# Kernel tuning notes

Measured on AMD Instinct MI355X. Metric: run time of the kernel, lower is better.

## Reference

```python
import jax, jax.numpy as jnp
import numpy as np

B = 50000      # batch of graphs
NOBJ = 7       # tangram pieces per graph
HID = 64
EMB = 32
SIGMA = 25.0   # VE-SDE sigma for marginal_prob_std


def _lin_init(k, fin, fout):
    kw, kb = jax.random.split(k)
    s = 1.0 / np.sqrt(fin)
    w = jax.random.uniform(kw, (fin, fout), minval=-s, maxval=s, dtype=jnp.float32)
    b = jax.random.uniform(kb, (fout,), minval=-s, maxval=s, dtype=jnp.float32)
    return w, b


def setup_inputs() -> dict:
    key = jax.random.key(0)
    ks = jax.random.split(key, 16)
    N = B * NOBJ
    omega = jax.random.normal(ks[0], (N, 3), dtype=jnp.float32)
    t = jax.random.uniform(ks[1], (B, 1), minval=1e-3, maxval=1.0, dtype=jnp.float32)
    # fully-connected edges (no self loops) per graph, offset by graph index
    a, b = np.meshgrid(np.arange(NOBJ), np.arange(NOBJ), indexing='ij')
    m = a != b
    src0, dst0 = a[m], b[m]                       # (42,)
    offs = (np.arange(B) * NOBJ)[:, None]         # (B,1)
    src = (src0[None, :] + offs).reshape(-1)
    dst = (dst0[None, :] + offs).reshape(-1)
    edge_index = jnp.asarray(np.stack([src, dst]), dtype=jnp.int32)  # (2, B*42)
    W_fourier = jax.random.normal(ks[2], (EMB // 2,), dtype=jnp.float32) * 30.0
    wi1, bi1 = _lin_init(ks[3], 3, HID)
    wi2, bi2 = _lin_init(ks[4], HID, HID)
    wt, bt = _lin_init(ks[5], EMB, EMB)
    w1a, b1a = _lin_init(ks[6], HID * 2, HID)
    w1b, b1b = _lin_init(ks[7], HID, HID)
    w2a, b2a = _lin_init(ks[8], (HID + EMB) * 2, HID)
    w2b, b2b = _lin_init(ks[9], HID, HID)
    w3a, b3a = _lin_init(ks[10], (HID + EMB) * 2, HID)
    w3b, b3b = _lin_init(ks[11], HID, 3)
    return dict(omega=omega, edge_index=edge_index, t=t, num_objs=NOBJ,
                W_fourier=W_fourier,
                wi1=wi1, bi1=bi1, wi2=wi2, bi2=bi2, wt=wt, bt=bt,
                w1a=w1a, b1a=b1a, w1b=w1b, b1b=b1b,
                w2a=w2a, b2a=b2a, w2b=w2b, b2b=b2b,
                w3a=w3a, b3a=b3a, w3b=w3b, b3b=b3b)


def _mlp(x, wa, ba, wb, bb):
    return jax.nn.relu(x @ wa + ba) @ wb + bb


def reference(omega, edge_index, t, num_objs, W_fourier,
              wi1, bi1, wi2, bi2, wt, bt,
              w1a, b1a, w1b, b1b, w2a, b2a, w2b, b2b, w3a, b3a, w3b, b3b):
    N = omega.shape[0]
    src, dst = edge_index[0], edge_index[1]

    def edge_conv(x, wa, ba, wb, bb):
        # EdgeConv: msg = mlp([x_i, x_j - x_i]); max-aggregate at target i
        xi = x[dst]
        msg = _mlp(jnp.concatenate([xi, x[src] - xi], axis=-1), wa, ba, wb, bb)
        return jax.ops.segment_max(msg, dst, num_segments=N)

    init_feature = _mlp(omega, wi1, bi1, wi2, bi2)          # (N, HID)
    # Gaussian Fourier time embedding -> ReLU -> Linear -> ReLU
    proj = t[:, 0][:, None] * W_fourier[None, :] * (2.0 * jnp.pi)   # (B, EMB/2)
    emb = jnp.concatenate([jnp.sin(proj), jnp.cos(proj)], axis=-1)  # (B, EMB)
    xs = jax.nn.relu(jax.nn.relu(emb) @ wt + bt)                    # (B, EMB)
    # torch: xs.repeat(1, num_objs, 1).view(B*num_objs, -1) == tile whole block
    x_sigma = jnp.tile(xs, (num_objs, 1))                           # (N, EMB)

    x = jax.nn.relu(edge_conv(init_feature, w1a, b1a, w1b, b1b))
    x = jnp.concatenate([x, x_sigma], axis=-1)
    x = jax.nn.relu(edge_conv(x, w2a, b2a, w2b, b2b))
    x = jnp.concatenate([x, x_sigma], axis=-1)
    x = edge_conv(x, w3a, b3a, w3b, b3b)                            # (N, 3)

    # torch: t.repeat(1, num_objs).view(B*num_objs, -1) == repeat_interleave
    t_r = jnp.repeat(t, num_objs, axis=0)                           # (N, 1)
    std = jnp.sqrt((SIGMA ** (2.0 * t_r) - 1.0) / (2.0 * jnp.log(SIGMA)))
    return x / (std + 1e-7)
```

## Files before the change

### kernel.cpp

```cpp
#include <hip/hip_runtime.h>


#define NB 50000

typedef unsigned short u16;
typedef unsigned int u32;
typedef short short8 __attribute__((ext_vector_type(8)));
typedef float f32x4 __attribute__((ext_vector_type(4)));
typedef unsigned int u32x4 __attribute__((ext_vector_type(4)));

#define OFF_I  0
#define OFF_1A 8192
#define OFF_2A 24576
#define OFF_3A 49152
#define OFF_1B 73728
#define OFF_2B 81920
#define OFF_WT 90112
#define OFF_3B 92160

#define HSTR 144
#define HLO  2304
#define PQS  304
#define SOFF 8512
#define SSTR 264
#define WREG 12736

__device__ __forceinline__ float b2f(u16 u) {
    return __uint_as_float(((u32)u) << 16);
}
__device__ __forceinline__ u16 f2b(float f) {
    u32 u = __float_as_uint(f);
    u += 0x7FFFu + ((u >> 16) & 1u);
    return (u16)(u >> 16);
}
__device__ __forceinline__ void split2(float v, u16& h, u16& l) {
    u32 u = __float_as_uint(v);
    h = (u16)(u >> 16);
    float d = v - __uint_as_float(u & 0xffff0000u);
    l = f2b(d);
}
__device__ __forceinline__ float bcast(float v, int l) {
    return __uint_as_float(__builtin_amdgcn_readlane(__float_as_uint(v), l));
}

__global__ __launch_bounds__(128) void pack_kernel(
    const float* __restrict__ wi2, const float* __restrict__ w1a,
    const float* __restrict__ w2a, const float* __restrict__ w3a,
    const float* __restrict__ w1b, const float* __restrict__ w2b,
    const float* __restrict__ wt,  const float* __restrict__ w3b,
    u16* __restrict__ ws)
{
    int blk = blockIdx.x;
    int j    = blockIdx.y;
    int half = threadIdx.x >> 6;
    int lane = threadIdx.x & 63;
    float v;
    u16* dst;
    if (blk < 88) {
        const float* src; int NT, qoff, obase, frag;
        if (blk < 8)       { src = wi2; NT = 4; qoff = 0;  obase = OFF_I;  frag = blk;      }
        else if (blk < 24) { src = w1a; NT = 8; qoff = 64; obase = OFF_1A; frag = blk - 8;  }
        else if (blk < 48) { src = w2a; NT = 8; qoff = 96; obase = OFF_2A; frag = blk - 24; }
        else if (blk < 72) { src = w3a; NT = 8; qoff = 96; obase = OFF_3A; frag = blk - 48; }
        else if (blk < 80) { src = w1b; NT = 4; qoff = 0;  obase = OFF_1B; frag = blk - 72; }
        else               { src = w2b; NT = 4; qoff = 0;  obase = OFF_2B; frag = blk - 80; }
        int kt = frag / NT, nt = frag % NT;
        int k = kt * 32 + (lane >> 4) * 8 + j;
        int n = nt * 16 + (lane & 15);
        int idx = (n < 64) ? (k * 64 + n) : ((qoff + k) * 64 + (n - 64));
        v = src[idx];
        dst = ws + obase + frag * 1024 + half * 512 + lane * 8 + j;
    } else if (blk < 90) {
        int frag = blk - 88;
        int k = (lane >> 4) * 8 + j;
        int n = frag * 16 + (lane & 15);
        v = wt[k * 32 + n];
        dst = ws + OFF_WT + frag * 1024 + half * 512 + lane * 8 + j;
    } else {
        int frag = blk - 90;
        int k = frag * 32 + (lane >> 4) * 8 + j;
        int n = lane & 15;
        v = (n < 3) ? w3b[k * 3 + n] : 0.f;
        dst = ws + OFF_3B + frag * 1024 + half * 512 + lane * 8 + j;
    }
    u16 hi = f2b(v);
    *dst = (half == 0) ? hi : f2b(v - b2f(hi));
}

__device__ __forceinline__ f32x4 mfma1(short8 a, short8 b, f32x4 acc) {
    return __builtin_amdgcn_mfma_f32_16x16x32_bf16(a, b, acc, 0, 0, 0);
}
__device__ __forceinline__ f32x4 mfma3(short8 ah, short8 al, short8 bh, short8 bl, f32x4 acc) {
    acc = mfma1(ah, bh, acc);
    acc = mfma1(ah, bl, acc);
    acc = mfma1(al, bh, acc);
    return acc;
}

#define ROW(k) ((k) < 7 ? (k) : (k) + 1)

__device__ __forceinline__ void putX(char* G, int k, int L, float v) {
    int r = ROW(k);
    u16 h, l;
    split2(v, h, l);
    *(u16*)(G + r * HSTR + L * 2) = h;
    *(u16*)(G + HLO + r * HSTR + L * 2) = l;
}
__device__ __forceinline__ void loadA2(const char* G, int L, short8* Ah, short8* Al) {
#pragma unroll
    for (int kt = 0; kt < 2; ++kt) {
        Ah[kt] = *(const short8*)(G + (L & 15) * HSTR + kt * 64 + (L >> 4) * 16);
        Al[kt] = *(const short8*)(G + HLO + (L & 15) * HSTR + kt * 64 + (L >> 4) * 16);
    }
}
template<int KT, int NT>
__device__ __forceinline__ void lin_pass(const u16* __restrict__ ws, int off, int nt0,
                                         const short8* Ah, const short8* Al,
                                         char* Sg, int L) {
#pragma unroll
    for (int ntc = 0; ntc < 4; ++ntc) {
        f32x4 a1 = {0.f, 0.f, 0.f, 0.f}, a2 = {0.f, 0.f, 0.f, 0.f};
#pragma unroll
        for (int kt = 0; kt < KT; ++kt) {
            int f = kt * NT + nt0 + ntc;
            short8 bh = *(const short8*)(ws + off + f * 1024 + L * 8);
            short8 bl = *(const short8*)(ws + off + f * 1024 + 512 + L * 8);
            a1 = mfma1(Ah[kt], bh, a1);
            a2 = mfma1(Ah[kt], bl, a2);
            a2 = mfma1(Al[kt], bh, a2);
        }
#pragma unroll
        for (int rr = 0; rr < 4; ++rr)
            *(float*)(Sg + ((L >> 4) * 4 + rr) * SSTR + ntc * 64 + (L & 15) * 4) = a1[rr] + a2[rr];
    }
}
__device__ __forceinline__ void copyQ(char* PQ, const char* Sb, int L) {
#pragma unroll
    for (int k = 0; k < 14; ++k)
        *(float*)(PQ + (14 + k) * PQS + L * 4) =
            *(const float*)(Sb + ROW(k) * SSTR + L * 4);
}
__device__ __forceinline__ void fixP(char* PQ, const char* Sb, float vb, int L) {
#pragma unroll
    for (int k = 0; k < 14; ++k) {
        float p = *(const float*)(Sb + ROW(k) * SSTR + L * 4);
        float q = *(const float*)(PQ + (14 + k) * PQS + L * 4);
        *(float*)(PQ + k * PQS + L * 4) = p + vb - q;
    }
}
__device__ __forceinline__ void pack2(float a, float b, u32& H, u32& Lo) {
    u32 ua = __float_as_uint(a), ub = __float_as_uint(b);
    H = __builtin_amdgcn_perm(ub, ua, 0x07060302);
    float da = a - __uint_as_float(ua & 0xffff0000u);
    float db = b - __uint_as_float(ub & 0xffff0000u);
    u32 r;
    asm("v_cvt_pk_bf16_f32 %0, %1, %2" : "=v"(r) : "v"(da), "v"(db));
    Lo = r;
}
__device__ __forceinline__ void buildA1(const char* bp, const char* bq,
                                        short8& Ah, short8& Al) {
    f32x4 p0 = *(const f32x4*)bp,  p1 = *(const f32x4*)(bp + 16);
    f32x4 q0 = *(const f32x4*)bq,  q1 = *(const f32x4*)(bq + 16);
    float h0 = fmaxf(p0[0] + q0[0], 0.f), h1 = fmaxf(p0[1] + q0[1], 0.f);
    float h2 = fmaxf(p0[2] + q0[2], 0.f), h3 = fmaxf(p0[3] + q0[3], 0.f);
    float h4 = fmaxf(p1[0] + q1[0], 0.f), h5 = fmaxf(p1[1] + q1[1], 0.f);
    float h6 = fmaxf(p1[2] + q1[2], 0.f), h7 = fmaxf(p1[3] + q1[3], 0.f);
    u32 H0, H1, H2, H3, L0, L1, L2, L3;
    pack2(h0, h1, H0, L0);
    pack2(h2, h3, H1, L1);
    pack2(h4, h5, H2, L2);
    pack2(h6, h7, H3, L3);
    u32x4 Hv = {H0, H1, H2, H3};
    u32x4 Lv = {L0, L1, L2, L3};
    Ah = __builtin_bit_cast(short8, Hv);
    Al = __builtin_bit_cast(short8, Lv);
}
__device__ __forceinline__ void buildA(const char* PQ, int c, int L,
                                       short8& Ah0, short8& Al0,
                                       short8& Ah1, short8& Al1) {
    int e  = c * 16 + (L & 15);
    int gb = (e >= 42) ? 1 : 0;
    int el = e - gb * 42;
    int i  = el / 6;
    int jj = el - i * 6;
    int j  = jj + (jj >= i);
    const char* bp = PQ + (gb * 7 + i) * PQS + (L >> 4) * 32;
    const char* bq = PQ + (14 + gb * 7 + j) * PQS + (L >> 4) * 32;
    buildA1(bp,       bq,       Ah0, Al0);
    buildA1(bp + 128, bq + 128, Ah1, Al1);
}
__device__ __forceinline__ void maxread(const char* Sb, int cc, float* mx, int L) {
#pragma unroll
    for (int r = 0; r < 16; ++r) {
        int e = cc * 16 + r;
        if (e < 84) {
            int gb = (e >= 42) ? 1 : 0;
            int i = (e - gb * 42) / 6;
            float sv = *(const float*)(Sb + r * SSTR + L * 4);
            mx[gb * 7 + i] = fmaxf(mx[gb * 7 + i], sv);
        }
    }
}

__device__ __forceinline__ void edgeconv_pipe(const u16* __restrict__ ws, int offB,
                                              char* W, char* Sb, float vb, int L) {
    const char* PQ = W;
    float mx[14];
#pragma unroll
    for (int k = 0; k < 14; ++k) mx[k] = -3.0e38f;
    short8 Ah0, Ah1, Al0, Al1;
    buildA(PQ, 0, L, Ah0, Al0, Ah1, Al1);
#pragma unroll
    for (int c = 0; c < 6; ++c) {
        if (c > 0) maxread(Sb, c - 1, mx, L);
#pragma unroll
        for (int nt = 0; nt < 4; ++nt) {
            short8 bh0 = *(const short8*)(ws + offB + nt * 1024 + L * 8);
            short8 bl0 = *(const short8*)(ws + offB + nt * 1024 + 512 + L * 8);
            short8 bh1 = *(const short8*)(ws + offB + (4 + nt) * 1024 + L * 8);
            short8 bl1 = *(const short8*)(ws + offB + (4 + nt) * 1024 + 512 + L * 8);
            f32x4 a1 = {0.f, 0.f, 0.f, 0.f}, a2 = {0.f, 0.f, 0.f, 0.f};
            a1 = mfma1(Ah0, bh0, a1);
            a2 = mfma1(Ah0, bl0, a2);
            a2 = mfma1(Al0, bh0, a2);
            a1 = mfma1(Ah1, bh1, a1);
            a2 = mfma1(Ah1, bl1, a2);
            a2 = mfma1(Al1, bh1, a2);
#pragma unroll
            for (int rr = 0; rr < 4; ++rr)
                *(float*)(Sb + ((L >> 4) * 4 + rr) * SSTR + nt * 64 + (L & 15) * 4) = a1[rr] + a2[rr];
        }
        if (c < 5) buildA(PQ, c + 1, L, Ah0, Al0, Ah1, Al1);
    }
    maxread(Sb, 5, mx, L);
#pragma unroll
    for (int k = 0; k < 14; ++k)
        putX(W, k, L, fmaxf(mx[k] + vb, 0.f));
}

__global__ __launch_bounds__(128, 3) void gnn_kernel(
    const float* __restrict__ omega, const float* __restrict__ tt, const float* __restrict__ Wf,
    const float* __restrict__ wi1, const float* __restrict__ bi1, const float* __restrict__ bi2,
    const float* __restrict__ bt,
    const float* __restrict__ b1a, const float* __restrict__ b1b,
    const float* __restrict__ b2a, const float* __restrict__ b2b,
    const float* __restrict__ b3a, const float* __restrict__ b3b,
    const u16* __restrict__ ws, float* __restrict__ out)
{
    __shared__ __align__(16) char smem[2 * WREG];
    const int L   = threadIdx.x & 63;
    const int wav = threadIdx.x >> 6;
    const int p   = blockIdx.x * 2 + wav;
    const int g0  = p * 2;
    const int base0 = g0 * 7;
    char* W   = smem + wav * WREG;
    char* Sb  = W + SOFF;

    float omv = (L < 42) ? omega[base0 * 3 + L] : 0.f;
    float vwi10 = wi1[L], vwi11 = wi1[64 + L], vwi12 = wi1[128 + L];
    float vbi1 = bi1[L];

    short8 Ah2, Al2;
    {
        int cc = L & 31;
        float vwf = Wf[cc & 15] * 6.283185307179586f;
        int tb = base0 - (base0 / NB) * NB;
#pragma unroll
        for (int k = 0; k < 14; ++k) {
            int ti = tb + k; if (ti >= NB) ti -= NB;
            float pj = tt[ti] * vwf;
            float remb = fmaxf((cc < 16) ? __sinf(pj) : __cosf(pj), 0.f);
            u16 h, l;
            split2(remb, h, l);
            if (L < 32) *(u16*)(W + ROW(k) * HSTR + cc * 2) = h;
            else *(u16*)(W + HLO + ROW(k) * HSTR + cc * 2) = l;
        }
        short8 Eh = *(const short8*)(W + (L & 15) * HSTR + (L >> 4) * 16);
        short8 El = *(const short8*)(W + HLO + (L & 15) * HSTR + (L >> 4) * 16);
#pragma unroll
        for (int nt = 0; nt < 2; ++nt) {
            short8 bh = *(const short8*)(ws + OFF_WT + nt * 1024 + L * 8);
            short8 bl = *(const short8*)(ws + OFF_WT + nt * 1024 + 512 + L * 8);
            f32x4 acc = {0.f, 0.f, 0.f, 0.f};
            acc = mfma3(Eh, El, bh, bl, acc);
#pragma unroll
            for (int rr = 0; rr < 4; ++rr)
                *(float*)(Sb + ((L >> 4) * 4 + rr) * SSTR + nt * 64 + (L & 15) * 4) = acc[rr];
        }
        float vbt = bt[cc];
#pragma unroll
        for (int k = 0; k < 14; ++k) {
            float xv = fmaxf(*(const float*)(Sb + ROW(k) * SSTR + cc * 4) + vbt, 0.f);
            u16 h, l;
            split2(xv, h, l);
            if (L < 32) *(u16*)(W + ROW(k) * HSTR + cc * 2) = h;
            else *(u16*)(W + HLO + ROW(k) * HSTR + cc * 2) = l;
        }
        Ah2 = *(const short8*)(W + (L & 15) * HSTR + (L >> 4) * 16);
        Al2 = *(const short8*)(W + HLO + (L & 15) * HSTR + (L >> 4) * 16);
    }

    short8 Ah[3], Al[3];

#pragma unroll
    for (int k = 0; k < 14; ++k) {
        float a0 = bcast(omv, 3 * k), a1 = bcast(omv, 3 * k + 1), a2 = bcast(omv, 3 * k + 2);
        putX(W, k, L, fmaxf(fmaf(a0, vwi10, fmaf(a1, vwi11, fmaf(a2, vwi12, vbi1))), 0.f));
    }

    loadA2(W, L, Ah, Al);
    lin_pass<2, 4>(ws, OFF_I, 0, Ah, Al, Sb, L);
    {
        float vbi2 = bi2[L];
#pragma unroll
        for (int k = 0; k < 14; ++k)
            putX(W, k, L, *(const float*)(Sb + ROW(k) * SSTR + L * 4) + vbi2);
    }

    loadA2(W, L, Ah, Al);
    lin_pass<2, 8>(ws, OFF_1A, 4, Ah, Al, Sb, L);
    copyQ(W, Sb, L);
    lin_pass<2, 8>(ws, OFF_1A, 0, Ah, Al, Sb, L);
    fixP(W, Sb, b1a[L], L);
    edgeconv_pipe(ws, OFF_1B, W, Sb, b1b[L], L);

    loadA2(W, L, Ah, Al);
    Ah[2] = Ah2; Al[2] = Al2;
    lin_pass<3, 8>(ws, OFF_2A, 4, Ah, Al, Sb, L);
    copyQ(W, Sb, L);
    lin_pass<3, 8>(ws, OFF_2A, 0, Ah, Al, Sb, L);
    fixP(W, Sb, b2a[L], L);
    edgeconv_pipe(ws, OFF_2B, W, Sb, b2b[L], L);

    loadA2(W, L, Ah, Al);
    Ah[2] = Ah2; Al[2] = Al2;
    lin_pass<3, 8>(ws, OFF_3A, 4, Ah, Al, Sb, L);
    copyQ(W, Sb, L);
    lin_pass<3, 8>(ws, OFF_3A, 0, Ah, Al, Sb, L);
    fixP(W, Sb, b3a[L], L);

    {
        const char* PQ = W;
        short8 B0h = *(const short8*)(ws + OFF_3B + L * 8);
        short8 B0l = *(const short8*)(ws + OFF_3B + 512 + L * 8);
        short8 B1h = *(const short8*)(ws + OFF_3B + 1024 + L * 8);
        short8 B1l = *(const short8*)(ws + OFF_3B + 1536 + L * 8);
        short8 Ah0, Ah1, Al0, Al1;
        buildA(PQ, 0, L, Ah0, Al0, Ah1, Al1);
#pragma unroll
        for (int c = 0; c < 6; ++c) {
            f32x4 a1 = {0.f, 0.f, 0.f, 0.f}, a2 = {0.f, 0.f, 0.f, 0.f};
            a1 = mfma1(Ah0, B0h, a1);
            a2 = mfma1(Ah0, B0l, a2);
            a2 = mfma1(Al0, B0h, a2);
            a1 = mfma1(Ah1, B1h, a1);
            a2 = mfma1(Ah1, B1l, a2);
            a2 = mfma1(Al1, B1h, a2);
            if ((L & 15) < 3) {
#pragma unroll
                for (int rr = 0; rr < 4; ++rr)
                    *(float*)(Sb + (c * 16 + (L >> 4) * 4 + rr) * 16 + (L & 15) * 4) = a1[rr] + a2[rr];
            }
            if (c < 5) buildA(PQ, c + 1, L, Ah0, Al0, Ah1, Al1);
        }
        if (L < 42) {
            int gb = (L >= 21) ? 1 : 0;
            int ll = L - gb * 21;
            int i = ll / 3, col = ll - i * 3;
            int e0 = gb * 42 + i * 6;
            float m = -3.0e38f;
#pragma unroll
            for (int e6 = 0; e6 < 6; ++e6)
                m = fmaxf(m, *(const float*)(Sb + (e0 + e6) * 16 + col * 4));
            m += b3b[col];
            float tg = tt[g0 + gb];
            float stdv = sqrtf((exp2f(tg * 9.287712379549448f) - 1.0f) * 0.15533740282828987f);
            out[base0 * 3 + L] = m / (stdv + 1e-7f);
        }
    }
}

extern "C" void kernel_launch(void* const* d_in, const int* in_sizes, int n_in,
                              void* d_out, int out_size, void* d_ws, size_t ws_size,
                              hipStream_t stream) {
    const float* omega = (const float*)d_in[0];
    const float* tt  = (const float*)d_in[2];
    const float* Wf  = (const float*)d_in[4];
    const float* wi1 = (const float*)d_in[5];
    const float* bi1 = (const float*)d_in[6];
    const float* wi2 = (const float*)d_in[7];
    const float* bi2 = (const float*)d_in[8];
    const float* wt  = (const float*)d_in[9];
    const float* bt  = (const float*)d_in[10];
    const float* w1a = (const float*)d_in[11];
    const float* b1a = (const float*)d_in[12];
    const float* w1b = (const float*)d_in[13];
    const float* b1b = (const float*)d_in[14];
    const float* w2a = (const float*)d_in[15];
    const float* b2a = (const float*)d_in[16];
    const float* w2b = (const float*)d_in[17];
    const float* b2b = (const float*)d_in[18];
    const float* w3a = (const float*)d_in[19];
    const float* b3a = (const float*)d_in[20];
    const float* w3b = (const float*)d_in[21];
    const float* b3b = (const float*)d_in[22];
    u16* ws = (u16*)d_ws;

    pack_kernel<<<dim3(92, 8), dim3(128), 0, stream>>>(wi2, w1a, w2a, w3a, w1b, w2b, wt, w3b, ws);
    gnn_kernel<<<dim3(12500), dim3(128), 0, stream>>>(
        omega, tt, Wf, wi1, bi1, bi2, bt,
        b1a, b1b, b2a, b2b, b3a, b3b, ws, (float*)d_out);
}
```

Baseline: 395.9 us.

## Cut VGPR pressure by parking long-lived values in AGPRs and streaming max

Moves the time-embedding A fragments, which live across the whole kernel, into accumulation registers (AGPRs) and reads them back only when needed. The per-node max reduction in edge conv now keeps one running carry instead of 14 live accumulators, stashing each finished max in AGPRs. The final-layer B weight fragments are reloaded inside the loop instead of being held live. The aim is lower VGPR pressure, avoiding spills or allowing higher occupancy, at the cost of extra accvgpr moves and repeated global loads.

```diff
diff --git a/kernel.cpp b/kernel.cpp
--- a/kernel.cpp
+++ b/kernel.cpp
@@ -41,6 +41,26 @@
 }
 __device__ __forceinline__ float bcast(float v, int l) {
     return __uint_as_float(__builtin_amdgcn_readlane(__float_as_uint(v), l));
+}
+__device__ __forceinline__ u32 toA(u32 v) {
+    u32 a;
+    asm("v_accvgpr_write_b32 %0, %1" : "=a"(a) : "v"(v));
+    return a;
+}
+__device__ __forceinline__ u32 frA(u32 a) {
+    u32 v;
+    asm("v_accvgpr_read_b32 %0, %1" : "=v"(v) : "a"(a));
+    return v;
+}
+__device__ __forceinline__ float toAf(float v) {
+    float a;
+    asm("v_accvgpr_write_b32 %0, %1" : "=a"(a) : "v"(v));
+    return a;
+}
+__device__ __forceinline__ float frAf(float a) {
+    float v;
+    asm("v_accvgpr_read_b32 %0, %1" : "=v"(v) : "a"(a));
+    return v;
 }
 
 __global__ __launch_bounds__(128) void pack_kernel(
@@ -189,15 +209,18 @@
     buildA1(bp,       bq,       Ah0, Al0);
     buildA1(bp + 128, bq + 128, Ah1, Al1);
 }
-__device__ __forceinline__ void maxread(const char* Sb, int cc, float* mx, int L) {
+__device__ __forceinline__ void foldS(const char* Sb, int cc, float* mA,
+                                      float& carry, int L) {
 #pragma unroll
     for (int r = 0; r < 16; ++r) {
         int e = cc * 16 + r;
         if (e < 84) {
-            int gb = (e >= 42) ? 1 : 0;
-            int i = (e - gb * 42) / 6;
+            int k = (e < 42) ? e / 6 : 7 + (e - 42) / 6;
+            int efirst = (k < 7) ? k * 6 : 42 + (k - 7) * 6;
             float sv = *(const float*)(Sb + r * SSTR + L * 4);
-            mx[gb * 7 + i] = fmaxf(mx[gb * 7 + i], sv);
+            if (e == efirst) carry = sv;
+            else carry = fmaxf(carry, sv);
+            if (e == efirst + 5) mA[k] = toAf(carry);
         }
     }
 }
@@ -205,14 +228,13 @@
 __device__ __forceinline__ void edgeconv_pipe(const u16* __restrict__ ws, int offB,
                                               char* W, char* Sb, float vb, int L) {
     const char* PQ = W;
-    float mx[14];
-#pragma unroll
-    for (int k = 0; k < 14; ++k) mx[k] = -3.0e38f;
+    float mA[14];
+    float carry = 0.f;
     short8 Ah0, Ah1, Al0, Al1;
     buildA(PQ, 0, L, Ah0, Al0, Ah1, Al1);
 #pragma unroll
     for (int c = 0; c < 6; ++c) {
-        if (c > 0) maxread(Sb, c - 1, mx, L);
+        if (c > 0) foldS(Sb, c - 1, mA, carry, L);
 #pragma unroll
         for (int nt = 0; nt < 4; ++nt) {
             short8 bh0 = *(const short8*)(ws + offB + nt * 1024 + L * 8);
@@ -232,10 +254,10 @@
         }
         if (c < 5) buildA(PQ, c + 1, L, Ah0, Al0, Ah1, Al1);
     }
-    maxread(Sb, 5, mx, L);
+    foldS(Sb, 5, mA, carry, L);
 #pragma unroll
     for (int k = 0; k < 14; ++k)
-        putX(W, k, L, fmaxf(mx[k] + vb, 0.f));
+        putX(W, k, L, fmaxf(frAf(mA[k]) + vb, 0.f));
 }
 
 __global__ __launch_bounds__(128, 3) void gnn_kernel(
@@ -260,7 +282,7 @@
     float vwi10 = wi1[L], vwi11 = wi1[64 + L], vwi12 = wi1[128 + L];
     float vbi1 = bi1[L];
 
-    short8 Ah2, Al2;
+    u32 xa0, xa1, xa2, xa3, xb0, xb1, xb2, xb3;
     {
         int cc = L & 31;
         float vwf = Wf[cc & 15] * 6.283185307179586f;
@@ -296,8 +318,12 @@
             if (L < 32) *(u16*)(W + ROW(k) * HSTR + cc * 2) = h;
             else *(u16*)(W + HLO + ROW(k) * HSTR + cc * 2) = l;
         }
-        Ah2 = *(const short8*)(W + (L & 15) * HSTR + (L >> 4) * 16);
-        Al2 = *(const short8*)(W + HLO + (L & 15) * HSTR + (L >> 4) * 16);
+        u32x4 hu = __builtin_bit_cast(u32x4,
+            *(const short8*)(W + (L & 15) * HSTR + (L >> 4) * 16));
+        u32x4 lu = __builtin_bit_cast(u32x4,
+            *(const short8*)(W + HLO + (L & 15) * HSTR + (L >> 4) * 16));
+        xa0 = toA(hu.x); xa1 = toA(hu.y); xa2 = toA(hu.z); xa3 = toA(hu.w);
+        xb0 = toA(lu.x); xb1 = toA(lu.y); xb2 = toA(lu.z); xb3 = toA(lu.w);
     }
 
     short8 Ah[3], Al[3];
@@ -325,7 +351,12 @@
     edgeconv_pipe(ws, OFF_1B, W, Sb, b1b[L], L);
 
     loadA2(W, L, Ah, Al);
-    Ah[2] = Ah2; Al[2] = Al2;
+    {
+        u32x4 hu = {frA(xa0), frA(xa1), frA(xa2), frA(xa3)};
+        u32x4 lu = {frA(xb0), frA(xb1), frA(xb2), frA(xb3)};
+        Ah[2] = __builtin_bit_cast(short8, hu);
+        Al[2] = __builtin_bit_cast(short8, lu);
+    }
     lin_pass<3, 8>(ws, OFF_2A, 4, Ah, Al, Sb, L);
     copyQ(W, Sb, L);
     lin_pass<3, 8>(ws, OFF_2A, 0, Ah, Al, Sb, L);
@@ -333,7 +364,12 @@
     edgeconv_pipe(ws, OFF_2B, W, Sb, b2b[L], L);
 
     loadA2(W, L, Ah, Al);
-    Ah[2] = Ah2; Al[2] = Al2;
+    {
+        u32x4 hu = {frA(xa0), frA(xa1), frA(xa2), frA(xa3)};
+        u32x4 lu = {frA(xb0), frA(xb1), frA(xb2), frA(xb3)};
+        Ah[2] = __builtin_bit_cast(short8, hu);
+        Al[2] = __builtin_bit_cast(short8, lu);
+    }
     lin_pass<3, 8>(ws, OFF_3A, 4, Ah, Al, Sb, L);
     copyQ(W, Sb, L);
     lin_pass<3, 8>(ws, OFF_3A, 0, Ah, Al, Sb, L);
@@ -341,14 +377,14 @@
 
     {
         const char* PQ = W;
-        short8 B0h = *(const short8*)(ws + OFF_3B + L * 8);
-        short8 B0l = *(const short8*)(ws + OFF_3B + 512 + L * 8);
-        short8 B1h = *(const short8*)(ws + OFF_3B + 1024 + L * 8);
-        short8 B1l = *(const short8*)(ws + OFF_3B + 1536 + L * 8);
         short8 Ah0, Ah1, Al0, Al1;
         buildA(PQ, 0, L, Ah0, Al0, Ah1, Al1);
 #pragma unroll
         for (int c = 0; c < 6; ++c) {
+            short8 B0h = *(const short8*)(ws + OFF_3B + L * 8);
+            short8 B0l = *(const short8*)(ws + OFF_3B + 512 + L * 8);
+            short8 B1h = *(const short8*)(ws + OFF_3B + 1024 + L * 8);
+            short8 B1l = *(const short8*)(ws + OFF_3B + 1536 + L * 8);
             f32x4 a1 = {0.f, 0.f, 0.f, 0.f}, a2 = {0.f, 0.f, 0.f, 0.f};
             a1 = mfma1(Ah0, B0h, a1);
             a2 = mfma1(Ah0, B0l, a2);
```

Result: slower. 416.0 us (+5.1%).
